# Performance work log

Measured on AMD Instinct MI355X. Metric: run time of the kernel, lower is better.

The kernel has to match this reference:

```python
import jax, jax.numpy as jnp
import numpy as np

B, T, C = 4, 2048, 1024
NH, NKV, HD = 16, 8, 64
K_ACTIVE = 8          # moh_active_heads_ratio 0.5 * 16 heads
VG = 32               # ve_gate input channels
EPS = 1e-6


def rms_norm(x):
    # F.rms_norm over last dim, no learned weight
    return x * jax.lax.rsqrt(jnp.mean(x * x, axis=-1, keepdims=True) + EPS)


def apply_rotary(x, cos, sin):
    # x: (B,T,H,HD); cos/sin: (1,T,1,HD//2)
    d = x.shape[-1] // 2
    x1, x2 = x[..., :d], x[..., d:]
    return jnp.concatenate([x1 * cos + x2 * sin, -x1 * sin + x2 * cos], axis=-1)


def setup_inputs() -> dict:
    key = jax.random.key(0)
    ks = jax.random.split(key, 9)
    x = jax.random.normal(ks[0], (B, T, C), dtype=jnp.float32)
    ve = jax.random.normal(ks[1], (B, T, NKV * HD), dtype=jnp.float32)
    # real rotary tables
    half = HD // 2
    inv_freq = 1.0 / (10000.0 ** (jnp.arange(half, dtype=jnp.float32) / half))
    ang = jnp.arange(T, dtype=jnp.float32)[:, None] * inv_freq[None, :]
    cos = jnp.cos(ang)[None, :, None, :]
    sin = jnp.sin(ang)[None, :, None, :]
    s = 0.02
    Wq = s * jax.random.normal(ks[2], (NH * HD, C), dtype=jnp.float32)
    Wk = s * jax.random.normal(ks[3], (NKV * HD, C), dtype=jnp.float32)
    Wv = s * jax.random.normal(ks[4], (NKV * HD, C), dtype=jnp.float32)
    Wo = s * jax.random.normal(ks[5], (C, C), dtype=jnp.float32)
    Wr = s * jax.random.normal(ks[6], (NH, C), dtype=jnp.float32)
    Wg = s * jax.random.normal(ks[7], (NKV, VG), dtype=jnp.float32)
    return {"x": x, "ve": ve, "cos": cos, "sin": sin, "Wq": Wq, "Wk": Wk,
            "Wv": Wv, "Wo": Wo, "Wr": Wr, "Wg": Wg, "window_size": 0}


def reference(x, ve, cos, sin, Wq, Wk, Wv, Wo, Wr, Wg, window_size):
    # head router: top-k binary mask per token (B,T,NH)
    logits = jnp.einsum('btc,hc->bth', x, Wr)
    topv = jax.lax.top_k(logits, K_ACTIVE)[0]
    head_mask = (logits >= topv[..., -1:]).astype(x.dtype)

    q = jnp.einsum('btc,dc->btd', x, Wq).reshape(B, T, NH, HD)
    k = jnp.einsum('btc,dc->btd', x, Wk).reshape(B, T, NKV, HD)
    v = jnp.einsum('btc,dc->btd', x, Wv).reshape(B, T, NKV, HD)

    # value-embedding gating
    gate = 2.0 * jax.nn.sigmoid(jnp.einsum('btg,kg->btk', x[..., :VG], Wg))  # (B,T,NKV)
    v = v + gate[..., None] * ve.reshape(B, T, NKV, HD)

    q = rms_norm(apply_rotary(q, cos, sin))
    k = rms_norm(apply_rotary(k, cos, sin))

    # GQA: repeat kv heads to NH
    rep = NH // NKV
    kr = jnp.repeat(k, rep, axis=2)  # (B,T,NH,HD)
    vr = jnp.repeat(v, rep, axis=2)

    scale = 1.0 / np.sqrt(HD)
    scores = jnp.einsum('bthd,bshd->bhts', q, kr) * scale  # (B,NH,T,T)
    causal = jnp.tril(jnp.ones((T, T), dtype=bool))
    scores = jnp.where(causal[None, None], scores, -jnp.inf)
    attn = jax.nn.softmax(scores, axis=-1)
    y = jnp.einsum('bhts,bshd->bthd', attn, vr)  # (B,T,NH,HD)

    y = y * head_mask[..., None]
    out = jnp.einsum('btd,cd->btc', y.reshape(B, T, C), Wo)
    return out, head_mask
```

## Files before the change

### kernel.cpp

```cpp
#include <hip/hip_runtime.h>
#include <math.h>

#define B_ 4
#define T_ 2048
#define C_ 1024
#define NH_ 16
#define NKV_ 8
#define HD_ 64
#define KACT_ 8
#define VG_ 32
#define EPS_ 1e-6f
#define LOG2E_ 1.44269504088896340736f

typedef __attribute__((ext_vector_type(8))) short bf16x8;
typedef __attribute__((ext_vector_type(4))) float f32x4;
typedef __attribute__((ext_vector_type(4))) unsigned short u16x4;
typedef unsigned short u16;
typedef unsigned int u32;

__device__ inline u16 f2bf(float f) {
    u32 u = __float_as_uint(f);
    u += 0x7fffu + ((u >> 16) & 1u);
    return (u16)(u >> 16);
}

__device__ inline u16 f2bf_t(float f) {
    return (u16)(__float_as_uint(f) >> 16);
}

__device__ inline float fast_exp2(float x) {
    float r;
    asm("v_exp_f32 %0, %1" : "=v"(r) : "v"(x));
    return r;
}

__device__ inline void gload_lds16(const void* g, void* s) {
    __builtin_amdgcn_global_load_lds((const __attribute__((address_space(1))) void*)g,
                                     (__attribute__((address_space(3))) void*)s, 16, 0, 0);
}

__device__ inline void bar() {
    asm volatile("" ::: "memory");
    __builtin_amdgcn_s_barrier();
    asm volatile("" ::: "memory");
}

__device__ inline int swz(int b) { return b ^ (((b >> 9) & 1) << 5); }

__global__ __launch_bounds__(256) void cast_weights_kernel(
    const float* __restrict__ Wq, const float* __restrict__ Wk,
    const float* __restrict__ Wv, const float* __restrict__ Wo,
    u16* __restrict__ wqkv, u16* __restrict__ wo)
{
    int i = blockIdx.x * 256 + threadIdx.x;
    const float* src; u16* dst; int j;
    if (i < 262144)      { src = Wq; dst = wqkv;           j = i; }
    else if (i < 393216) { src = Wk; dst = wqkv + 1048576; j = i - 262144; }
    else if (i < 524288) { src = Wv; dst = wqkv + 1572864; j = i - 393216; }
    else                 { src = Wo; dst = wo;             j = i - 524288; }
    float4 v = ((const float4*)src)[j];
    u16x4 o = { f2bf(v.x), f2bf(v.y), f2bf(v.z), f2bf(v.w) };
    ((u16x4*)dst)[j] = o;
}

template<int MODE>
__global__ __launch_bounds__(512) void gemm_bf16_256(
    const u16* __restrict__ A, const u16* __restrict__ W,
    float* __restrict__ Out, int M, int N, int K,
    float* __restrict__ q_out, float* __restrict__ k_out, u16* __restrict__ vT_out,
    const float* __restrict__ gate, const float* __restrict__ ve)
{
    __shared__ __align__(16) u16 AL[3][2][128 * 64];
    __shared__ __align__(16) u16 BL[2][128 * 64];
    const int tid = threadIdx.x;
    const int lane = tid & 63;
    const int w = tid >> 6;
    const int bm = blockIdx.y * 256;
    const int bn = blockIdx.x * 128;
    const int wm = (w >> 2) * 128;
    const int wn = (w & 3) * 32;
    const int ah = w >> 2;
    const int lr = lane & 15, lg = lane >> 4;
    const int NKT = K >> 6;

    f32x4 acc[8][2];
    #pragma unroll
    for (int mi = 0; mi < 8; ++mi)
        #pragma unroll
        for (int ni = 0; ni < 2; ++ni) acc[mi][ni] = f32x4{0.f, 0.f, 0.f, 0.f};

    auto stageA = [&](int kt) {
        const int db = kt % 3;
        #pragma unroll
        for (int hf = 0; hf < 2; ++hf)
            #pragma unroll
            for (int ci = 0; ci < 2; ++ci) {
                int c = tid + ci * 512;
                int l = c ^ (((c >> 5) & 1) << 1);
                gload_lds16(A + (size_t)(bm + hf * 128 + (l >> 3)) * K + kt * 64 + (l & 7) * 8,
                            (char*)&AL[db][hf][0] + c * 16);
            }
    };
    auto stageB = [&](int kt) {
        const int db = kt & 1;
        #pragma unroll
        for (int ci = 0; ci < 2; ++ci) {
            int c = tid + ci * 512;
            int l = c ^ (((c >> 5) & 1) << 1);
            gload_lds16(W + (size_t)(bn + (l >> 3)) * K + kt * 64 + (l & 7) * 8,
                        (char*)&BL[db][0] + c * 16);
        }
    };

    stageA(0);
    stageB(0);
    stageA(1);

    for (int kt = 0; kt < NKT; ++kt) {
        const int ab = kt % 3, bb = kt & 1;
        if (kt == NKT - 1) asm volatile("s_waitcnt vmcnt(0)" ::: "memory");
        else               asm volatile("s_waitcnt vmcnt(4)" ::: "memory");
        bar();
        #pragma unroll
        for (int ph = 0; ph < 2; ++ph) {
            bf16x8 af[4][2], bfm[2][2];
            #pragma unroll
            for (int mi2 = 0; mi2 < 4; ++mi2) {
                const int row = (ph * 4 + mi2) * 16 + lr;
                #pragma unroll
                for (int kk = 0; kk < 2; ++kk)
                    af[mi2][kk] = *(const bf16x8*)((const char*)&AL[ab][ah][0] +
                                                   swz(row * 128 + kk * 64 + lg * 16));
            }
            #pragma unroll
            for (int ni = 0; ni < 2; ++ni) {
                const int row = wn + ni * 16 + lr;
                #pragma unroll
                for (int kk = 0; kk < 2; ++kk)
                    bfm[ni][kk] = *(const bf16x8*)((const char*)&BL[bb][0] +
                                                   swz(row * 128 + kk * 64 + lg * 16));
            }
            if (ph == 0) { if (kt + 1 < NKT) stageB(kt + 1); }
            else         { if (kt + 2 < NKT) stageA(kt + 2); }
            bar();
            __builtin_amdgcn_s_setprio(1);
            #pragma unroll
            for (int mi2 = 0; mi2 < 4; ++mi2)
                #pragma unroll
                for (int ni = 0; ni < 2; ++ni)
                    #pragma unroll
                    for (int kk = 0; kk < 2; ++kk)
                        acc[ph * 4 + mi2][ni] = __builtin_amdgcn_mfma_f32_16x16x32_bf16(
                            af[mi2][kk], bfm[ni][kk], acc[ph * 4 + mi2][ni], 0, 0, 0);
            __builtin_amdgcn_s_setprio(0);
            bar();
        }
    }

    #pragma unroll
    for (int mi = 0; mi < 8; ++mi)
        #pragma unroll
        for (int ni = 0; ni < 2; ++ni) {
            const int row0 = bm + wm + mi * 16 + lg * 4;
            const int col = bn + wn + ni * 16 + lr;
            if (MODE == 0) {
                #pragma unroll
                for (int r = 0; r < 4; ++r)
                    Out[(size_t)(row0 + r) * N + col] = acc[mi][ni][r];
            } else {
                if (col < 1024) {
                    #pragma unroll
                    for (int r = 0; r < 4; ++r)
                        q_out[(size_t)(row0 + r) * 1024 + col] = acc[mi][ni][r];
                } else if (col < 1536) {
                    #pragma unroll
                    for (int r = 0; r < 4; ++r)
                        k_out[(size_t)(row0 + r) * 512 + (col - 1024)] = acc[mi][ni][r];
                } else {
                    const int cc = col - 1536;
                    const int kv = cc >> 6, d = cc & 63;
                    u16x4 pk;
                    #pragma unroll
                    for (int r = 0; r < 4; ++r) {
                        const int row = row0 + r;
                        pk[r] = f2bf(acc[mi][ni][r] +
                                     gate[row * NKV_ + kv] * ve[(size_t)row * 512 + cc]);
                    }
                    *(u16x4*)(vT_out + ((size_t)((row0 >> 11) * NKV_ + kv) * HD_ + d) * T_ +
                              (row0 & (T_ - 1))) = pk;
                }
            }
        }
}

__global__ __launch_bounds__(64) void logits_mask_gate_kernel(
    const float* __restrict__ x, const float* __restrict__ Wr,
    const float* __restrict__ Wg, float* __restrict__ hm, float* __restrict__ gate,
    u16* __restrict__ xb)
{
    const int token = blockIdx.x;
    const int lane = threadIdx.x;
    const float* xr = x + (size_t)token * C_;
    __shared__ float lg[NH_];
    __shared__ float thr_s;
    float part[NH_];
    #pragma unroll
    for (int h = 0; h < NH_; ++h) part[h] = 0.f;
    for (int c = lane; c < C_; c += 64) {
        float xv = xr[c];
        xb[(size_t)token * C_ + c] = f2bf(xv);
        #pragma unroll
        for (int h = 0; h < NH_; ++h) part[h] = fmaf(xv, Wr[h * C_ + c], part[h]);
    }
    #pragma unroll
    for (int h = 0; h < NH_; ++h) {
        float s = part[h];
        #pragma unroll
        for (int off = 32; off; off >>= 1) s += __shfl_xor(s, off);
        if (lane == 0) lg[h] = s;
    }
    __syncthreads();
    if (lane == 0) {
        unsigned used = 0;
        float last = 0.f;
        for (int p = 0; p < KACT_; ++p) {
            float bv = -3.4e38f; int bi = 0;
            for (int i = 0; i < NH_; ++i)
                if (!(used & (1u << i)) && lg[i] > bv) { bv = lg[i]; bi = i; }
            used |= 1u << bi;
            last = bv;
        }
        thr_s = last;
    }
    __syncthreads();
    if (lane < NH_) hm[(size_t)token * NH_ + lane] = (lg[lane] >= thr_s) ? 1.f : 0.f;
    if (lane < NKV_) {
        float s = 0.f;
        #pragma unroll
        for (int g = 0; g < VG_; ++g) s = fmaf(xr[g], Wg[lane * VG_ + g], s);
        gate[(size_t)token * NKV_ + lane] = 2.f / (1.f + __expf(-s));
    }
}

__global__ __launch_bounds__(256) void rope_rms_kernel(
    const float* __restrict__ src, int src_stride, u16* __restrict__ dst,
    const float* __restrict__ cosT, const float* __restrict__ sinT,
    int hshift, float scale)
{
    const int tid = threadIdx.x;
    const int vec = blockIdx.x * 16 + (tid >> 4);
    const int idx = tid & 15;
    const int heads = 1 << hshift;
    const int m = vec >> hshift;
    const int hh = vec & (heads - 1);
    const int t = m & (T_ - 1);
    const int bb = m >> 11;
    const float4 v4 = *(const float4*)(src + (size_t)m * src_stride + hh * 64 + idx * 4);
    const float4 c4 = *(const float4*)(cosT + t * 32 + (idx & 7) * 4);
    const float4 s4 = *(const float4*)(sinT + t * 32 + (idx & 7) * 4);
    const float p0 = __shfl_xor(v4.x, 8);
    const float p1 = __shfl_xor(v4.y, 8);
    const float p2 = __shfl_xor(v4.z, 8);
    const float p3 = __shfl_xor(v4.w, 8);
    float r0, r1, r2, r3;
    if (idx < 8) {
        r0 = fmaf(v4.x, c4.x, p0 * s4.x); r1 = fmaf(v4.y, c4.y, p1 * s4.y);
        r2 = fmaf(v4.z, c4.z, p2 * s4.z); r3 = fmaf(v4.w, c4.w, p3 * s4.w);
    } else {
        r0 = fmaf(v4.x, c4.x, -p0 * s4.x); r1 = fmaf(v4.y, c4.y, -p1 * s4.y);
        r2 = fmaf(v4.z, c4.z, -p2 * s4.z); r3 = fmaf(v4.w, c4.w, -p3 * s4.w);
    }
    float ss = fmaf(r0, r0, fmaf(r1, r1, fmaf(r2, r2, r3 * r3)));
    ss += __shfl_xor(ss, 1);
    ss += __shfl_xor(ss, 2);
    ss += __shfl_xor(ss, 4);
    ss += __shfl_xor(ss, 8);
    const float sc = rsqrtf(ss * (1.0f / HD_) + EPS_) * scale;
    u16x4 o = { f2bf(r0 * sc), f2bf(r1 * sc), f2bf(r2 * sc), f2bf(r3 * sc) };
    *(u16x4*)(dst + ((size_t)(bb * heads + hh) * T_ + t) * HD_ + idx * 4) = o;
}

__global__ __launch_bounds__(512) void attn_mfma_kernel(
    const u16* __restrict__ qb, const u16* __restrict__ kb,
    const u16* __restrict__ vbT, const float* __restrict__ hm,
    u16* __restrict__ yb)
{
    __shared__ __align__(16) u16 Ks[64 * 72];
    __shared__ __align__(16) u16 Vt[64 * 72];
    __shared__ __align__(16) u16 Ps[8 * 16 * 72];
    const int bid = blockIdx.x;
    const int qblk = 15 - (bid >> 6);
    const int b = (bid >> 4) & 3;
    const int h = bid & 15;
    const int kv = h >> 1;
    const int tid = threadIdx.x;
    const int lane = tid & 63;
    const int w = tid >> 6;
    const int lr = lane & 15;
    const int lg = lane >> 4;
    const int q0 = qblk * 128;
    const int qt_max = 2 * qblk + 1;

    bf16x8 qf[2];
    {
        const u16* src = qb + ((size_t)(b * NH_ + h) * T_ + q0 + w * 16 + lr) * HD_ + lg * 8;
        qf[0] = *(const bf16x8*)(src);
        qf[1] = *(const bf16x8*)(src + 32);
    }
    f32x4 yacc[4];
    #pragma unroll
    for (int dt = 0; dt < 4; ++dt) yacc[dt] = f32x4{0.f, 0.f, 0.f, 0.f};
    float m = -1e30f, l = 0.f;

    const u16* kbase = kb + (size_t)(b * NKV_ + kv) * T_ * HD_;
    const u16* vbase = vbT + ((size_t)(b * NKV_) + kv) * (size_t)HD_ * T_;
    u16* Pw = Ps + w * 16 * 72;
    const int qrow_g = q0 + w * 16 + lr;

    const int a0 = tid >> 3, g0 = tid & 7;
    bf16x8 kreg, vreg;
    auto LOADT = [&](int kt) {
        kreg = *(const bf16x8*)(kbase + (size_t)(kt * 64 + a0) * HD_ + g0 * 8);
        vreg = *(const bf16x8*)(vbase + (size_t)a0 * T_ + kt * 64 + g0 * 8);
    };
    auto WRITET = [&]() {
        *(bf16x8*)&Ks[a0 * 72 + g0 * 8] = kreg;
        *(bf16x8*)&Vt[a0 * 72 + g0 * 8] = vreg;
    };

    LOADT(0);
    WRITET();
    for (int kt = 0; kt <= qt_max; ++kt) {
        __syncthreads();
        if (kt < qt_max) LOADT(kt + 1);
        const int rel = q0 + w * 16 + 15 - kt * 64;
        if (rel >= 0) {
            const int mtmax = min(3, rel >> 4);
            f32x4 st[4];
            #pragma unroll
            for (int mt = 0; mt < 4; ++mt) st[mt] = f32x4{0.f, 0.f, 0.f, 0.f};
            __builtin_amdgcn_s_setprio(1);
            #pragma unroll
            for (int mt = 0; mt < 4; ++mt) {
                if (mt <= mtmax) {
                    bf16x8 kf0 = *(const bf16x8*)&Ks[(mt * 16 + lr) * 72 + lg * 8];
                    bf16x8 kf1 = *(const bf16x8*)&Ks[(mt * 16 + lr) * 72 + lg * 8 + 32];
                    st[mt] = __builtin_amdgcn_mfma_f32_16x16x32_bf16(kf0, qf[0], st[mt], 0, 0, 0);
                    st[mt] = __builtin_amdgcn_mfma_f32_16x16x32_bf16(kf1, qf[1], st[mt], 0, 0, 0);
                }
            }
            __builtin_amdgcn_s_setprio(0);
            float smax = -1e30f;
            #pragma unroll
            for (int mt = 0; mt < 4; ++mt) {
                #pragma unroll
                for (int r = 0; r < 4; ++r) {
                    int keyg = kt * 64 + mt * 16 + lg * 4 + r;
                    float s = (mt <= mtmax && keyg <= qrow_g) ? st[mt][r] : -1e30f;
                    st[mt][r] = s;
                    smax = fmaxf(smax, s);
                }
            }
            smax = fmaxf(smax, __shfl_xor(smax, 16));
            smax = fmaxf(smax, __shfl_xor(smax, 32));
            if (!__all(smax <= m + 8.f)) {
                const float mnew = fmaxf(m, smax);
                const float corr = fast_exp2(m - mnew);
                l *= corr;
                float cr[4];
                #pragma unroll
                for (int r = 0; r < 4; ++r) cr[r] = __shfl(corr, lg * 4 + r);
                #pragma unroll
                for (int dt = 0; dt < 4; ++dt)
                    #pragma unroll
                    for (int r = 0; r < 4; ++r) yacc[dt][r] *= cr[r];
                m = mnew;
            }
            float psum = 0.f;
            #pragma unroll
            for (int mt = 0; mt < 4; ++mt) {
                float p0 = fast_exp2(st[mt][0] - m);
                float p1 = fast_exp2(st[mt][1] - m);
                float p2 = fast_exp2(st[mt][2] - m);
                float p3 = fast_exp2(st[mt][3] - m);
                psum += (p0 + p1) + (p2 + p3);
                u16x4 pk = { f2bf_t(p0), f2bf_t(p1), f2bf_t(p2), f2bf_t(p3) };
                *(u16x4*)&Pw[lr * 72 + mt * 16 + lg * 4] = pk;
            }
            psum += __shfl_xor(psum, 16);
            psum += __shfl_xor(psum, 32);
            l += psum;
            const int kimax = min(1, rel >> 5);
            __builtin_amdgcn_s_setprio(1);
            #pragma unroll
            for (int ki = 0; ki < 2; ++ki) {
                if (ki <= kimax) {
                    bf16x8 pf = *(const bf16x8*)&Pw[lr * 72 + ki * 32 + lg * 8];
                    #pragma unroll
                    for (int dt = 0; dt < 4; ++dt) {
                        bf16x8 vf = *(const bf16x8*)&Vt[(dt * 16 + lr) * 72 + ki * 32 + lg * 8];
                        yacc[dt] = __builtin_amdgcn_mfma_f32_16x16x32_bf16(pf, vf, yacc[dt], 0, 0, 0);
                    }
                }
            }
            __builtin_amdgcn_s_setprio(0);
        }
        __syncthreads();
        if (kt < qt_max) WRITET();
    }
    const float linv = 1.f / l;
    #pragma unroll
    for (int r = 0; r < 4; ++r) {
        const float lrv = __shfl(linv, lg * 4 + r);
        const int t = q0 + w * 16 + lg * 4 + r;
        const float hmv = hm[((size_t)(b * T_) + t) * NH_ + h];
        const float sc = lrv * hmv;
        #pragma unroll
        for (int dt = 0; dt < 4; ++dt)
            yb[(((size_t)(b * T_) + t) * NH_ + h) * HD_ + dt * 16 + lr] = f2bf(yacc[dt][r] * sc);
    }
}

extern "C" void kernel_launch(void* const* d_in, const int* in_sizes, int n_in,
                              void* d_out, int out_size, void* d_ws, size_t ws_size,
                              hipStream_t stream) {
    const float* x    = (const float*)d_in[0];
    const float* ve   = (const float*)d_in[1];
    const float* cosT = (const float*)d_in[2];
    const float* sinT = (const float*)d_in[3];
    const float* Wq   = (const float*)d_in[4];
    const float* Wk   = (const float*)d_in[5];
    const float* Wv   = (const float*)d_in[6];
    const float* Wo   = (const float*)d_in[7];
    const float* Wr   = (const float*)d_in[8];
    const float* Wg   = (const float*)d_in[9];
    float* out = (float*)d_out;
    float* hm  = out + (size_t)B_ * T_ * C_;

    const int M = B_ * T_;
    float* ws = (float*)d_ws;
    float* qf32  = ws;
    float* kf32  = qf32 + 8388608;
    float* xbr   = kf32 + 4194304;
    float* wqkvr = xbr + 4194304;
    float* wor   = wqkvr + 1048576;
    float* gate  = wor + 524288;
    float* vtr   = gate + 65536;
    float* kbr   = vtr + 2097152;

    u16* xb    = (u16*)xbr;
    u16* Wqkvb = (u16*)wqkvr;
    u16* Wob   = (u16*)wor;
    u16* vbT   = (u16*)vtr;
    u16* qb    = (u16*)xbr;
    u16* kb    = (u16*)kbr;
    u16* yb    = (u16*)qf32;

    cast_weights_kernel<<<3072, 256, 0, stream>>>(Wq, Wk, Wv, Wo, Wqkvb, Wob);
    logits_mask_gate_kernel<<<M, 64, 0, stream>>>(x, Wr, Wg, hm, gate, xb);
    gemm_bf16_256<1><<<dim3(2048 / 128, M / 256), 512, 0, stream>>>(
        xb, Wqkvb, nullptr, M, 2048, C_, qf32, kf32, vbT, gate, ve);
    rope_rms_kernel<<<(M * NH_) / 16, 256, 0, stream>>>(qf32, 1024, qb, cosT, sinT, 4, 0.125f * LOG2E_);
    rope_rms_kernel<<<(M * NKV_) / 16, 256, 0, stream>>>(kf32, 512, kb, cosT, sinT, 3, 1.0f);
    attn_mfma_kernel<<<B_ * NH_ * (T_ / 128), 512, 0, stream>>>(qb, kb, vbT, hm, yb);
    gemm_bf16_256<0><<<dim3(C_ / 128, M / 256), 512, 0, stream>>>(
        yb, Wob, out, M, C_, C_, nullptr, nullptr, nullptr, nullptr, nullptr);
}
```

Before: 222.5 us.

## Use dedicated 256x256-tile GEMM for the fused QKV projection

Adds a separate QKV projection kernel with 256x256 output tiles, each wave computing 128x64, and double-buffered LDS for A and B. The previous version used 256x128 tiles. The larger tile is meant to raise arithmetic intensity and cut redundant A-tile loads from global memory. The trade-off is fewer blocks: the grid drops from 512 to 256, which is about one block per CU on the 256-CU MI355X. It also raises accumulator register pressure (32 f32x4 per thread) and uses 128KB of LDS, which can limit occupancy and latency hiding. The output GEMM keeps the old kernel with the QKV epilogue removed.

Result: slower. 257.3 us (+15.6%).

```diff
diff --git a/kernel.cpp b/kernel.cpp
--- a/kernel.cpp
+++ b/kernel.cpp
@@ -63,12 +63,121 @@
     ((u16x4*)dst)[j] = o;
 }
 
+__global__ __launch_bounds__(512) void gemm_qkv_256x256(
+    const u16* __restrict__ A, const u16* __restrict__ W, int M, int K,
+    float* __restrict__ q_out, float* __restrict__ k_out, u16* __restrict__ vT_out,
+    const float* __restrict__ gate, const float* __restrict__ ve)
+{
+    __shared__ __align__(16) u16 AL[2][256 * 64];
+    __shared__ __align__(16) u16 BL[2][256 * 64];
+    const int tid = threadIdx.x;
+    const int lane = tid & 63;
+    const int w = tid >> 6;
+    const int bm = blockIdx.y * 256;
+    const int bn = blockIdx.x * 256;
+    const int wm = (w >> 2) * 128;
+    const int wn = (w & 3) * 64;
+    const int lr = lane & 15, lg = lane >> 4;
+    const int NKT = K >> 6;
+
+    f32x4 acc[8][4];
+    #pragma unroll
+    for (int mi = 0; mi < 8; ++mi)
+        #pragma unroll
+        for (int ni = 0; ni < 4; ++ni) acc[mi][ni] = f32x4{0.f, 0.f, 0.f, 0.f};
+
+    auto stageA = [&](int kt) {
+        const int db = kt & 1;
+        #pragma unroll
+        for (int ci = 0; ci < 4; ++ci) {
+            int c = tid + ci * 512;
+            int l = c ^ (((c >> 5) & 1) << 1);
+            gload_lds16(A + (size_t)(bm + (l >> 3)) * K + kt * 64 + (l & 7) * 8,
+                        (char*)&AL[db][0] + c * 16);
+        }
+    };
+    auto stageB = [&](int kt) {
+        const int db = kt & 1;
+        #pragma unroll
+        for (int ci = 0; ci < 4; ++ci) {
+            int c = tid + ci * 512;
+            int l = c ^ (((c >> 5) & 1) << 1);
+            gload_lds16(W + (size_t)(bn + (l >> 3)) * K + kt * 64 + (l & 7) * 8,
+                        (char*)&BL[db][0] + c * 16);
+        }
+    };
+
+    stageA(0);
+    stageB(0);
+    for (int kt = 0; kt < NKT; ++kt) {
+        const int db = kt & 1;
+        asm volatile("s_waitcnt vmcnt(0)" ::: "memory");
+        bar();
+        bf16x8 af[8][2], bfm[4][2];
+        #pragma unroll
+        for (int mi = 0; mi < 8; ++mi) {
+            const int row = wm + mi * 16 + lr;
+            #pragma unroll
+            for (int kk = 0; kk < 2; ++kk)
+                af[mi][kk] = *(const bf16x8*)((const char*)&AL[db][0] +
+                                              swz(row * 128 + kk * 64 + lg * 16));
+        }
+        #pragma unroll
+        for (int ni = 0; ni < 4; ++ni) {
+            const int row = wn + ni * 16 + lr;
+            #pragma unroll
+            for (int kk = 0; kk < 2; ++kk)
+                bfm[ni][kk] = *(const bf16x8*)((const char*)&BL[db][0] +
+                                               swz(row * 128 + kk * 64 + lg * 16));
+        }
+        if (kt + 1 < NKT) { stageA(kt + 1); stageB(kt + 1); }
+        __builtin_amdgcn_s_setprio(1);
+        #pragma unroll
+        for (int mi = 0; mi < 8; ++mi)
+            #pragma unroll
+            for (int ni = 0; ni < 4; ++ni)
+                #pragma unroll
+                for (int kk = 0; kk < 2; ++kk)
+                    acc[mi][ni] = __builtin_amdgcn_mfma_f32_16x16x32_bf16(
+                        af[mi][kk], bfm[ni][kk], acc[mi][ni], 0, 0, 0);
+        __builtin_amdgcn_s_setprio(0);
+        bar();
+    }
+
+    #pragma unroll
+    for (int mi = 0; mi < 8; ++mi)
+        #pragma unroll
+        for (int ni = 0; ni < 4; ++ni) {
+            const int row0 = bm + wm + mi * 16 + lg * 4;
+            const int col = bn + wn + ni * 16 + lr;
+            if (col < 1024) {
+                #pragma unroll
+                for (int r = 0; r < 4; ++r)
+                    q_out[(size_t)(row0 + r) * 1024 + col] = acc[mi][ni][r];
+            } else if (col < 1536) {
+                #pragma unroll
+                for (int r = 0; r < 4; ++r)
+                    k_out[(size_t)(row0 + r) * 512 + (col - 1024)] = acc[mi][ni][r];
+            } else {
+                const int cc = col - 1536;
+                const int kv = cc >> 6, d = cc & 63;
+                u16x4 pk;
+                #pragma unroll
+                for (int r = 0; r < 4; ++r) {
+                    const int row = row0 + r;
+                    pk[r] = f2bf(acc[mi][ni][r] +
+                                 gate[row * NKV_ + kv] * ve[(size_t)row * 512 + cc]);
+                }
+                *(u16x4*)(vT_out + ((size_t)((row0 >> 11) * NKV_ + kv) * HD_ + d) * T_ +
+                          (row0 & (T_ - 1))) = pk;
+            }
+        }
+}
+
 template<int MODE>
 __global__ __launch_bounds__(512) void gemm_bf16_256(
     const u16* __restrict__ A, const u16* __restrict__ W,
-    float* __restrict__ Out, int M, int N, int K,
-    float* __restrict__ q_out, float* __restrict__ k_out, u16* __restrict__ vT_out,
-    const float* __restrict__ gate, const float* __restrict__ ve)
+    float* __restrict__ Out, int M, int N, int K)
 {
     __shared__ __align__(16) u16 AL[3][2][128 * 64];
     __shared__ __align__(16) u16 BL[2][128 * 64];
@@ -163,33 +272,9 @@
         for (int ni = 0; ni < 2; ++ni) {
             const int row0 = bm + wm + mi * 16 + lg * 4;
             const int col = bn + wn + ni * 16 + lr;
-            if (MODE == 0) {
-                #pragma unroll
-                for (int r = 0; r < 4; ++r)
-                    Out[(size_t)(row0 + r) * N + col] = acc[mi][ni][r];
-            } else {
-                if (col < 1024) {
-                    #pragma unroll
-                    for (int r = 0; r < 4; ++r)
-                        q_out[(size_t)(row0 + r) * 1024 + col] = acc[mi][ni][r];
-                } else if (col < 1536) {
-                    #pragma unroll
-                    for (int r = 0; r < 4; ++r)
-                        k_out[(size_t)(row0 + r) * 512 + (col - 1024)] = acc[mi][ni][r];
-                } else {
-                    const int cc = col - 1536;
-                    const int kv = cc >> 6, d = cc & 63;
-                    u16x4 pk;
-                    #pragma unroll
-                    for (int r = 0; r < 4; ++r) {
-                        const int row = row0 + r;
-                        pk[r] = f2bf(acc[mi][ni][r] +
-                                     gate[row * NKV_ + kv] * ve[(size_t)row * 512 + cc]);
-                    }
-                    *(u16x4*)(vT_out + ((size_t)((row0 >> 11) * NKV_ + kv) * HD_ + d) * T_ +
-                              (row0 & (T_ - 1))) = pk;
-                }
-            }
+            #pragma unroll
+            for (int r = 0; r < 4; ++r)
+                Out[(size_t)(row0 + r) * N + col] = acc[mi][ni][r];
         }
 }
 
@@ -458,11 +543,11 @@
 
     cast_weights_kernel<<<3072, 256, 0, stream>>>(Wq, Wk, Wv, Wo, Wqkvb, Wob);
     logits_mask_gate_kernel<<<M, 64, 0, stream>>>(x, Wr, Wg, hm, gate, xb);
-    gemm_bf16_256<1><<<dim3(2048 / 128, M / 256), 512, 0, stream>>>(
-        xb, Wqkvb, nullptr, M, 2048, C_, qf32, kf32, vbT, gate, ve);
+    gemm_qkv_256x256<<<dim3(2048 / 256, M / 256), 512, 0, stream>>>(
+        xb, Wqkvb, M, C_, qf32, kf32, vbT, gate, ve);
     rope_rms_kernel<<<(M * NH_) / 16, 256, 0, stream>>>(qf32, 1024, qb, cosT, sinT, 4, 0.125f * LOG2E_);
     rope_rms_kernel<<<(M * NKV_) / 16, 256, 0, stream>>>(kf32, 512, kb, cosT, sinT, 3, 1.0f);
     attn_mfma_kernel<<<B_ * NH_ * (T_ / 128), 512, 0, stream>>>(qb, kb, vbT, hm, yb);
     gemm_bf16_256<0><<<dim3(C_ / 128, M / 256), 512, 0, stream>>>(
-        yb, Wob, out, M, C_, C_, nullptr, nullptr, nullptr, nullptr, nullptr);
-}
+        yb, Wob, out, M, C_, C_);
+}
```
